# Kernel tuning notes

Hardware: AMD Instinct MI355X
Metric: run time of the kernel (lower is better)

The kernel has to match this reference:

```python
import math
import jax, jax.numpy as jnp
import numpy as np

B, T = 65536, 34
VOCAB, TOK_DIM, POS_DIM, D_MODEL, FFN_DIM, HEAD_DIM = 14, 2, 3, 5, 2, 5
EPS = 1e-5

def _pos_flat_idx():
    # replicate _build_pos_map: 10 digits, Z_HI, 10 digits, Z_HI, 10 digits, special0, special1
    sources, indices = [], []
    for _ in range(3):
        for i in range(10):
            sources.append(0); indices.append(i)
        sources.append(2); indices.append(len([s for s in sources if s == 2]) - 1)
    # fix: the torch code appends (2,0),(2,1) after first two digit blocks and (1,0),(2,2) after the third
    sources, indices = [], []
    for i in range(10): sources.append(0); indices.append(i)
    sources.append(2); indices.append(0)
    for i in range(10): sources.append(0); indices.append(i)
    sources.append(2); indices.append(1)
    for i in range(10): sources.append(0); indices.append(i)
    sources.append(1); indices.append(0)
    sources.append(2); indices.append(2)
    src = np.array(sources); idx = np.array(indices)
    # table layout: rows 0..9 digit_pos, row 10 z_hi_pos, rows 11..13 special (learned0, learned1, eos)
    offs = np.array([0, 10, 11])
    return offs[src] + idx  # (34,)

POS_FLAT = jnp.asarray(_pos_flat_idx())
CAUSAL = jnp.tril(jnp.ones((T, T), dtype=bool))

def _rms(x, w):
    return x * jax.lax.rsqrt(jnp.mean(x * x, -1, keepdims=True) + EPS) * w

def setup_inputs():
    key = jax.random.key(0)
    ks = jax.random.split(key, 16)
    n = lambda i, shape: jax.random.normal(ks[i], shape, jnp.float32) * 0.5
    return {
        'idx': jax.random.randint(ks[0], (B, T), 0, VOCAB),
        'tok_emb': n(1, (VOCAB, TOK_DIM)),
        'spiral_amp': jnp.float32(1.0),
        'spiral_phase': jnp.float32(0.1),
        'spiral_slope': jnp.float32(1.0 / 9.0),
        'spiral_offset': jnp.float32(0.05),
        'pos_corr_slope': jnp.float32(0.01),
        'pos_corr_intercept': jnp.float32(0.02),
        'z_hi_pos': n(2, (1, POS_DIM)),
        'special_pos': n(3, (2, POS_DIM)),
        'q_w': n(4, (HEAD_DIM, POS_DIM)),
        'v_w': n(5, (HEAD_DIM, TOK_DIM)),
        'out_A': n(6, (HEAD_DIM, 2)),
        'out_B': n(7, (2, D_MODEL)),
        'q_phase': n(8, (1,)),
        'ln1_w': jnp.ones((D_MODEL,), jnp.float32),
        'ln2_w': jnp.ones((D_MODEL,), jnp.float32),
        'lnf_w': jnp.ones((D_MODEL,), jnp.float32),
        'fc1_w': n(9, (FFN_DIM, D_MODEL)),
        'fc1_b': n(10, (FFN_DIM,)),
        'fc2_w': n(11, (D_MODEL, FFN_DIM)),
        'fc2_b': n(12, (D_MODEL,)),
        'head_w': n(13, (TOK_DIM, D_MODEL)),
    }

def reference(idx, tok_emb, spiral_amp, spiral_phase, spiral_slope, spiral_offset,
              pos_corr_slope, pos_corr_intercept, z_hi_pos, special_pos,
              q_w, v_w, out_A, out_B, q_phase, ln1_w, ln2_w, lnf_w,
              fc1_w, fc1_b, fc2_w, fc2_b, head_w):
    # learned spiral digit positions (10, 3)
    i = jnp.arange(10, dtype=jnp.float32)
    angle = 2.0 * math.pi * i / 10.0 + spiral_phase
    base = jnp.stack([spiral_amp * jnp.cos(angle),
                      spiral_amp * jnp.sin(angle),
                      spiral_slope * i + spiral_offset], -1)
    corr = pos_corr_intercept + pos_corr_slope * i
    digit_pos = base * (1.0 + corr)[:, None]
    table = jnp.concatenate([digit_pos, z_hi_pos, special_pos,
                             jnp.zeros((1, POS_DIM), jnp.float32)], 0)  # (14, 3)
    pos = table[POS_FLAT]  # (T, 3)

    tok = tok_emb[idx]  # (B, T, 2)
    x = jnp.concatenate([tok, jnp.broadcast_to(pos, (idx.shape[0], T, POS_DIM))], -1)  # (B,T,5)

    h = _rms(x, ln1_w)
    q = jnp.einsum('btp,dp->btd', h[..., TOK_DIM:], q_w)  # (B,T,5)
    k = q  # q_proj applied to same input for both q and k
    v = jnp.einsum('btp,dp->btd', h[..., :TOK_DIM], v_w)  # (B,T,5)

    # per-head 2D rotation on first 4 dims (HEAD_DIM//2 = 2 pairs), dim 4 unchanged
    c, s = jnp.cos(q_phase[0]), jnp.sin(q_phase[0])
    q0, q1 = q[..., 0:4:2], q[..., 1:4:2]
    q_rot = jnp.concatenate([
        jnp.stack([q0 * c - q1 * s, q0 * s + q1 * c], -1).reshape(q.shape[:-1] + (4,)),
        q[..., 4:]], -1)

    att = jnp.einsum('btd,bsd->bts', q_rot, k) / math.sqrt(HEAD_DIM)
    att = jnp.where(CAUSAL, att, -jnp.inf)
    att = jax.nn.softmax(att, -1)
    out = jnp.einsum('bts,bsd->btd', att, v)  # (B,T,5)

    x = x + (out @ out_A) @ out_B  # low-rank out_proj
    hh = _rms(x, ln2_w)
    x = x + (jax.nn.gelu(hh @ fc1_w.T + fc1_b, approximate=False) @ fc2_w.T + fc2_b)
    x = _rms(x, lnf_w)
    return (x @ head_w.T) @ tok_emb.T  # (B, T, 14)
```

## Files before the change

kernel.cpp:

```cpp
#include <hip/hip_runtime.h>
#include <math.h>

#define T_SEQ 34
#define NTOK 14
#define NE (T_SEQ * NTOK)
#define RPB 64
#define NWAVE 7

__global__ __launch_bounds__(448) void micro_fused_kernel(
    const int* __restrict__ idx,
    const float* __restrict__ tok_emb,
    const float* __restrict__ s_amp, const float* __restrict__ s_phase,
    const float* __restrict__ s_slope, const float* __restrict__ s_offset,
    const float* __restrict__ pc_slope, const float* __restrict__ pc_int,
    const float* __restrict__ z_hi, const float* __restrict__ spec,
    const float* __restrict__ q_w, const float* __restrict__ v_w,
    const float* __restrict__ out_A, const float* __restrict__ out_B,
    const float* __restrict__ q_phase,
    const float* __restrict__ ln1_w, const float* __restrict__ ln2_w,
    const float* __restrict__ lnf_w,
    const float* __restrict__ fc1_w, const float* __restrict__ fc1_b,
    const float* __restrict__ fc2_w, const float* __restrict__ fc2_b,
    const float* __restrict__ head_w,
    float* __restrict__ out, int N)
{
    __shared__ float2 HXY[NE];
    __shared__ float2 HZ0[NE];
    __shared__ float  H1s[NE];
    __shared__ float  C3x[NE], C3y[NE], C3z[NE];
    __shared__ float  PosX[T_SEQ], PosY[T_SEQ], PosZ[T_SEQ];
    __shared__ float  TE[NTOK * 2];
    __shared__ float  PMs[10];
    __shared__ float  Ws[5 * NTOK];
    __shared__ float  ln2s[5], lnfs[5], fc1ws[10], fc1bs[2], fc2ws[10], fc2bs[5];
    __shared__ int    toksT[T_SEQ * RPB];

    const int lane  = threadIdx.x;
    const int chunk = threadIdx.y;
    const int tid   = chunk * RPB + lane;

    {
        const float amp = s_amp[0], ph = s_phase[0], slp = s_slope[0], off = s_offset[0];
        const float pcs = pc_slope[0], pci = pc_int[0];
        const float cph = cosf(q_phase[0]), sph = sinf(q_phase[0]);
        const float escale = 0.44721359549995793f * 1.4426950408889634f;
        for (int e = tid; e < NE; e += 448) {
            int t = e / NTOK, tk = e - t * NTOK;
            float px, py, pz;
            if (t == 33)      { px = 0.f;     py = 0.f;     pz = 0.f; }
            else if (t == 32) { px = z_hi[0]; py = z_hi[1]; pz = z_hi[2]; }
            else if (t == 10) { px = spec[0]; py = spec[1]; pz = spec[2]; }
            else if (t == 21) { px = spec[3]; py = spec[4]; pz = spec[5]; }
            else {
                int i = (t < 10) ? t : (t < 21 ? t - 11 : t - 22);
                float fi = (float)i;
                float ang = 0.62831853071795864769f * fi + ph;
                float mlt = 1.f + pci + pcs * fi;
                px = amp * cosf(ang) * mlt;
                py = amp * sinf(ang) * mlt;
                pz = (slp * fi + off) * mlt;
            }
            if (tk == 0) { PosX[t] = px; PosY[t] = py; PosZ[t] = pz; }
            float x0 = tok_emb[tk * 2], x1 = tok_emb[tk * 2 + 1];
            float ssum = x0*x0 + x1*x1 + px*px + py*py + pz*pz;
            float r = rsqrtf(ssum * 0.2f + 1e-5f);
            float h0 = x0 * r * ln1_w[0], h1 = x1 * r * ln1_w[1];
            float h2 = px * r * ln1_w[2], h3 = py * r * ln1_w[3], h4 = pz * r * ln1_w[4];
            float q0 = q_w[0]  * h2 + q_w[1]  * h3 + q_w[2]  * h4;
            float q1 = q_w[3]  * h2 + q_w[4]  * h3 + q_w[5]  * h4;
            float q2 = q_w[6]  * h2 + q_w[7]  * h3 + q_w[8]  * h4;
            float q3 = q_w[9]  * h2 + q_w[10] * h3 + q_w[11] * h4;
            float q4 = q_w[12] * h2 + q_w[13] * h3 + q_w[14] * h4;
            float r0 = q0 * cph - q1 * sph, r1 = q0 * sph + q1 * cph;
            float r2c = q2 * cph - q3 * sph, r3 = q2 * sph + q3 * cph;
            C3x[e] = (r0*q_w[0] + r1*q_w[3] + r2c*q_w[6] + r3*q_w[9]  + q4*q_w[12]) * escale;
            C3y[e] = (r0*q_w[1] + r1*q_w[4] + r2c*q_w[7] + r3*q_w[10] + q4*q_w[13]) * escale;
            C3z[e] = (r0*q_w[2] + r1*q_w[5] + r2c*q_w[8] + r3*q_w[11] + q4*q_w[14]) * escale;
            HXY[e] = make_float2(h2, h3);
            HZ0[e] = make_float2(h4, h0);
            H1s[e] = h1;
        }
    }
    if (tid < 28) TE[tid] = tok_emb[tid];
    if (tid < 70) {
        int d = tid / NTOK, v = tid - d * NTOK;
        Ws[tid] = head_w[d] * tok_emb[v * 2] + head_w[5 + d] * tok_emb[v * 2 + 1];
    }
    if (tid < 10) {
        int j = tid >> 1, c = tid & 1;
        float acc = 0.f;
        for (int i = 0; i < 5; ++i) {
            float m5 = out_A[i*2] * out_B[j] + out_A[i*2+1] * out_B[5 + j];
            acc += m5 * v_w[i*2 + c];
        }
        PMs[tid] = acc;
    }
    if (tid < 5)  { ln2s[tid] = ln2_w[tid]; lnfs[tid] = lnf_w[tid]; fc2bs[tid] = fc2_b[tid]; }
    if (tid < 10) { fc1ws[tid] = fc1_w[tid]; fc2ws[tid] = fc2_w[tid]; }
    if (tid < 2)  { fc1bs[tid] = fc1_b[tid]; }

    const int Brows = N / T_SEQ;
    const int rowBase = blockIdx.x * RPB;
    for (int j = tid; j < RPB * T_SEQ; j += 448) {
        int r = j / T_SEQ, s = j - r * T_SEQ;
        int rr = rowBase + r;
        toksT[s * RPB + r] = (rr < Brows) ? idx[rr * T_SEQ + s] : 0;
    }
    __syncthreads();

    const int t_base  = chunk * 5;
    const int loop_end = (chunk == 6) ? 33 : (t_base + 4);

    float c3x[5], c3y[5], c3z[5], L[5], A0[5], A1[5];
#pragma unroll
    for (int j = 0; j < 5; ++j) {
        L[j] = 0.f; A0[j] = 0.f; A1[j] = 0.f;
        int t = t_base + j;
        if (t < T_SEQ) {
            int e = t * NTOK + toksT[t * RPB + lane];
            c3x[j] = C3x[e]; c3y[j] = C3y[e]; c3z[j] = C3z[e];
        } else { c3x[j] = 0.f; c3y[j] = 0.f; c3z[j] = 0.f; }
    }

    for (int s = 0; s < t_base; ++s) {
        int e = s * NTOK + toksT[s * RPB + lane];
        float2 hxy = HXY[e], hz0 = HZ0[e];
        float h1 = H1s[e];
#pragma unroll
        for (int j = 0; j < 5; ++j) {
            float sc = fmaf(c3x[j], hxy.x, fmaf(c3y[j], hxy.y, c3z[j] * hz0.x));
            float p = exp2f(sc);
            L[j] += p;
            A0[j] = fmaf(p, hz0.y, A0[j]);
            A1[j] = fmaf(p, h1, A1[j]);
        }
    }
    for (int s = t_base; s <= loop_end; ++s) {
        int e = s * NTOK + toksT[s * RPB + lane];
        float2 hxy = HXY[e], hz0 = HZ0[e];
        float h1 = H1s[e];
#pragma unroll
        for (int j = 0; j < 5; ++j) {
            if (s <= t_base + j) {
                float sc = fmaf(c3x[j], hxy.x, fmaf(c3y[j], hxy.y, c3z[j] * hz0.x));
                float p = exp2f(sc);
                L[j] += p;
                A0[j] = fmaf(p, hz0.y, A0[j]);
                A1[j] = fmaf(p, h1, A1[j]);
            }
        }
    }

    const int r = rowBase + lane;
    if (r >= Brows) return;
#pragma unroll
    for (int j = 0; j < 5; ++j) {
        int t = t_base + j;
        if (t < T_SEQ) {
            float il = 1.f / L[j];
            float a0 = A0[j] * il, a1 = A1[j] * il;
            int tok = toksT[t * RPB + lane];
            float xv0 = TE[tok * 2], xv1 = TE[tok * 2 + 1];
            float xv2 = PosX[t], xv3 = PosY[t], xv4 = PosZ[t];
            float y[5];
            y[0] = xv0 + PMs[0] * a0 + PMs[1] * a1;
            y[1] = xv1 + PMs[2] * a0 + PMs[3] * a1;
            y[2] = xv2 + PMs[4] * a0 + PMs[5] * a1;
            y[3] = xv3 + PMs[6] * a0 + PMs[7] * a1;
            y[4] = xv4 + PMs[8] * a0 + PMs[9] * a1;

            float s2 = y[0]*y[0] + y[1]*y[1] + y[2]*y[2] + y[3]*y[3] + y[4]*y[4];
            float r2 = rsqrtf(s2 * 0.2f + 1e-5f);
            float hh[5];
#pragma unroll
            for (int k = 0; k < 5; ++k) hh[k] = y[k] * r2 * ln2s[k];

            float u0 = fc1bs[0], u1 = fc1bs[1];
#pragma unroll
            for (int k = 0; k < 5; ++k) { u0 += hh[k] * fc1ws[k]; u1 += hh[k] * fc1ws[5 + k]; }
            float g0 = 0.5f * u0 * (1.f + erff(u0 * 0.70710678118654752f));
            float g1 = 0.5f * u1 * (1.f + erff(u1 * 0.70710678118654752f));

            float y2[5]; float s3 = 0.f;
#pragma unroll
            for (int k = 0; k < 5; ++k) {
                y2[k] = y[k] + g0 * fc2ws[k * 2] + g1 * fc2ws[k * 2 + 1] + fc2bs[k];
                s3 += y2[k] * y2[k];
            }
            float r3 = rsqrtf(s3 * 0.2f + 1e-5f);
            float z[5];
#pragma unroll
            for (int k = 0; k < 5; ++k) z[k] = y2[k] * r3 * lnfs[k];

            float res[14];
#pragma unroll
            for (int v = 0; v < 14; ++v)
                res[v] = z[0] * Ws[v] + z[1] * Ws[14 + v] + z[2] * Ws[28 + v]
                       + z[3] * Ws[42 + v] + z[4] * Ws[56 + v];

            float2* op = (float2*)(out + (size_t)(r * T_SEQ + t) * 14);
#pragma unroll
            for (int v = 0; v < 7; ++v) op[v] = make_float2(res[2 * v], res[2 * v + 1]);
        }
    }
}

extern "C" void kernel_launch(void* const* d_in, const int* in_sizes, int n_in,
                              void* d_out, int out_size, void* d_ws, size_t ws_size,
                              hipStream_t stream) {
    const int N = in_sizes[0];
    const int Brows = N / T_SEQ;
    dim3 block(RPB, NWAVE);
    dim3 grid((Brows + RPB - 1) / RPB);
    micro_fused_kernel<<<grid, block, 0, stream>>>(
        (const int*)d_in[0],
        (const float*)d_in[1], (const float*)d_in[2], (const float*)d_in[3],
        (const float*)d_in[4], (const float*)d_in[5], (const float*)d_in[6],
        (const float*)d_in[7], (const float*)d_in[8], (const float*)d_in[9],
        (const float*)d_in[10], (const float*)d_in[11], (const float*)d_in[12],
        (const float*)d_in[13], (const float*)d_in[14], (const float*)d_in[15],
        (const float*)d_in[16], (const float*)d_in[17], (const float*)d_in[18],
        (const float*)d_in[19], (const float*)d_in[20], (const float*)d_in[21],
        (const float*)d_in[22],
        (float*)d_out, N);
}
```

Baseline: 232.1 us.

## Stage attention results in shared memory and remap epilogue for coalesced output writes

The per-row attention outputs (a0, a1) are written to a padded row-major shared buffer that aliases the precompute tables. A second phase then remaps threads so consecutive threads handle consecutive (row, t) elements. Each warp's output stores become contiguous, where before each lane wrote a separate row's stride. The token matrix is also stored row-major with padding of 35 to avoid bank conflicts. This costs extra barriers and shared-memory traffic.

```diff
diff --git a/kernel.cpp b/kernel.cpp
--- a/kernel.cpp
+++ b/kernel.cpp
@@ -6,6 +6,7 @@
 #define NE (T_SEQ * NTOK)
 #define RPB 64
 #define NWAVE 7
+#define TPAD 35
 
 __global__ __launch_bounds__(448) void micro_fused_kernel(
     const int* __restrict__ idx,
@@ -24,16 +25,22 @@
     const float* __restrict__ head_w,
     float* __restrict__ out, int N)
 {
-    __shared__ float2 HXY[NE];
-    __shared__ float2 HZ0[NE];
-    __shared__ float  H1s[NE];
-    __shared__ float  C3x[NE], C3y[NE], C3z[NE];
-    __shared__ float  PosX[T_SEQ], PosY[T_SEQ], PosZ[T_SEQ];
-    __shared__ float  TE[NTOK * 2];
-    __shared__ float  PMs[10];
-    __shared__ float  Ws[5 * NTOK];
-    __shared__ float  ln2s[5], lnfs[5], fc1ws[10], fc1bs[2], fc2ws[10], fc2bs[5];
-    __shared__ int    toksT[T_SEQ * RPB];
+    __shared__ float SH[RPB * TPAD * 2];
+    __shared__ float PosX[T_SEQ], PosY[T_SEQ], PosZ[T_SEQ];
+    __shared__ float TE[NTOK * 2];
+    __shared__ float PMs[10];
+    __shared__ float Ws[5 * NTOK];
+    __shared__ float ln2s[5], lnfs[5], fc1ws[10], fc1bs[2], fc2ws[10], fc2bs[5];
+    __shared__ int   toksR[RPB * TPAD];
+
+    float2* HXY = (float2*)SH;
+    float2* HZ0 = (float2*)(SH + 952);
+    float*  H1s = SH + 1904;
+    float*  C3x = SH + 2380;
+    float*  C3y = SH + 2856;
+    float*  C3z = SH + 3332;
+    float*  A0s = SH;
+    float*  A1s = SH + RPB * TPAD;
 
     const int lane  = threadIdx.x;
     const int chunk = threadIdx.y;
@@ -104,12 +111,13 @@
     for (int j = tid; j < RPB * T_SEQ; j += 448) {
         int r = j / T_SEQ, s = j - r * T_SEQ;
         int rr = rowBase + r;
-        toksT[s * RPB + r] = (rr < Brows) ? idx[rr * T_SEQ + s] : 0;
+        toksR[r * TPAD + s] = (rr < Brows) ? idx[rr * T_SEQ + s] : 0;
     }
     __syncthreads();
 
-    const int t_base  = chunk * 5;
+    const int t_base   = chunk * 5;
     const int loop_end = (chunk == 6) ? 33 : (t_base + 4);
+    const int rowOff   = lane * TPAD;
 
     float c3x[5], c3y[5], c3z[5], L[5], A0[5], A1[5];
 #pragma unroll
@@ -117,13 +125,13 @@
         L[j] = 0.f; A0[j] = 0.f; A1[j] = 0.f;
         int t = t_base + j;
         if (t < T_SEQ) {
-            int e = t * NTOK + toksT[t * RPB + lane];
+            int e = t * NTOK + toksR[rowOff + t];
             c3x[j] = C3x[e]; c3y[j] = C3y[e]; c3z[j] = C3z[e];
         } else { c3x[j] = 0.f; c3y[j] = 0.f; c3z[j] = 0.f; }
     }
 
     for (int s = 0; s < t_base; ++s) {
-        int e = s * NTOK + toksT[s * RPB + lane];
+        int e = s * NTOK + toksR[rowOff + s];
         float2 hxy = HXY[e], hz0 = HZ0[e];
         float h1 = H1s[e];
 #pragma unroll
@@ -136,7 +144,7 @@
         }
     }
     for (int s = t_base; s <= loop_end; ++s) {
-        int e = s * NTOK + toksT[s * RPB + lane];
+        int e = s * NTOK + toksR[rowOff + s];
         float2 hxy = HXY[e], hz0 = HZ0[e];
         float h1 = H1s[e];
 #pragma unroll
@@ -151,57 +159,64 @@
         }
     }
 
-    const int r = rowBase + lane;
-    if (r >= Brows) return;
+    __syncthreads();
 #pragma unroll
     for (int j = 0; j < 5; ++j) {
         int t = t_base + j;
-        if (t < T_SEQ) {
-            float il = 1.f / L[j];
-            float a0 = A0[j] * il, a1 = A1[j] * il;
-            int tok = toksT[t * RPB + lane];
-            float xv0 = TE[tok * 2], xv1 = TE[tok * 2 + 1];
-            float xv2 = PosX[t], xv3 = PosY[t], xv4 = PosZ[t];
-            float y[5];
-            y[0] = xv0 + PMs[0] * a0 + PMs[1] * a1;
-            y[1] = xv1 + PMs[2] * a0 + PMs[3] * a1;
-            y[2] = xv2 + PMs[4] * a0 + PMs[5] * a1;
-            y[3] = xv3 + PMs[6] * a0 + PMs[7] * a1;
-            y[4] = xv4 + PMs[8] * a0 + PMs[9] * a1;
-
-            float s2 = y[0]*y[0] + y[1]*y[1] + y[2]*y[2] + y[3]*y[3] + y[4]*y[4];
-            float r2 = rsqrtf(s2 * 0.2f + 1e-5f);
-            float hh[5];
-#pragma unroll
-            for (int k = 0; k < 5; ++k) hh[k] = y[k] * r2 * ln2s[k];
-
-            float u0 = fc1bs[0], u1 = fc1bs[1];
-#pragma unroll
-            for (int k = 0; k < 5; ++k) { u0 += hh[k] * fc1ws[k]; u1 += hh[k] * fc1ws[5 + k]; }
-            float g0 = 0.5f * u0 * (1.f + erff(u0 * 0.70710678118654752f));
-            float g1 = 0.5f * u1 * (1.f + erff(u1 * 0.70710678118654752f));
-
-            float y2[5]; float s3 = 0.f;
-#pragma unroll
-            for (int k = 0; k < 5; ++k) {
-                y2[k] = y[k] + g0 * fc2ws[k * 2] + g1 * fc2ws[k * 2 + 1] + fc2bs[k];
-                s3 += y2[k] * y2[k];
-            }
-            float r3 = rsqrtf(s3 * 0.2f + 1e-5f);
-            float z[5];
-#pragma unroll
-            for (int k = 0; k < 5; ++k) z[k] = y2[k] * r3 * lnfs[k];
-
-            float res[14];
-#pragma unroll
-            for (int v = 0; v < 14; ++v)
-                res[v] = z[0] * Ws[v] + z[1] * Ws[14 + v] + z[2] * Ws[28 + v]
-                       + z[3] * Ws[42 + v] + z[4] * Ws[56 + v];
-
-            float2* op = (float2*)(out + (size_t)(r * T_SEQ + t) * 14);
-#pragma unroll
-            for (int v = 0; v < 7; ++v) op[v] = make_float2(res[2 * v], res[2 * v + 1]);
-        }
+        float il = 1.f / L[j];
+        int o = rowOff + ((t < TPAD) ? t : (TPAD - 1));
+        A0s[o] = A0[j] * il;
+        A1s[o] = A1[j] * il;
+    }
+    __syncthreads();
+
+    const int elemsPerBlock = RPB * T_SEQ;
+    for (int e0 = tid; e0 < elemsPerBlock; e0 += 448) {
+        int r = e0 / T_SEQ, t = e0 - r * T_SEQ;
+        size_t lin = (size_t)rowBase * T_SEQ + e0;
+        if (lin >= (size_t)N) break;
+        float a0 = A0s[r * TPAD + t];
+        float a1 = A1s[r * TPAD + t];
+        int tok = toksR[r * TPAD + t];
+        float y[5];
+        y[0] = TE[tok * 2]     + PMs[0] * a0 + PMs[1] * a1;
+        y[1] = TE[tok * 2 + 1] + PMs[2] * a0 + PMs[3] * a1;
+        y[2] = PosX[t] + PMs[4] * a0 + PMs[5] * a1;
+        y[3] = PosY[t] + PMs[6] * a0 + PMs[7] * a1;
+        y[4] = PosZ[t] + PMs[8] * a0 + PMs[9] * a1;
+
+        float s2 = y[0]*y[0] + y[1]*y[1] + y[2]*y[2] + y[3]*y[3] + y[4]*y[4];
+        float r2 = rsqrtf(s2 * 0.2f + 1e-5f);
+        float hh[5];
+#pragma unroll
+        for (int k = 0; k < 5; ++k) hh[k] = y[k] * r2 * ln2s[k];
+
+        float u0 = fc1bs[0], u1 = fc1bs[1];
+#pragma unroll
+        for (int k = 0; k < 5; ++k) { u0 += hh[k] * fc1ws[k]; u1 += hh[k] * fc1ws[5 + k]; }
+        float g0 = 0.5f * u0 * (1.f + erff(u0 * 0.70710678118654752f));
+        float g1 = 0.5f * u1 * (1.f + erff(u1 * 0.70710678118654752f));
+
+        float y2[5]; float s3 = 0.f;
+#pragma unroll
+        for (int k = 0; k < 5; ++k) {
+            y2[k] = y[k] + g0 * fc2ws[k * 2] + g1 * fc2ws[k * 2 + 1] + fc2bs[k];
+            s3 += y2[k] * y2[k];
+        }
+        float r3 = rsqrtf(s3 * 0.2f + 1e-5f);
+        float z[5];
+#pragma unroll
+        for (int k = 0; k < 5; ++k) z[k] = y2[k] * r3 * lnfs[k];
+
+        float res[14];
+#pragma unroll
+        for (int v = 0; v < 14; ++v)
+            res[v] = z[0] * Ws[v] + z[1] * Ws[14 + v] + z[2] * Ws[28 + v]
+                   + z[3] * Ws[42 + v] + z[4] * Ws[56 + v];
+
+        float2* op = (float2*)(out + lin * 14);
+#pragma unroll
+        for (int v = 0; v < 7; ++v) op[v] = make_float2(res[2 * v], res[2 * v + 1]);
     }
 }
 
```

Measured after the change: 240.4 us. 1.04x slower.
